# Performance work log

Measured on AMD Instinct MI355X. Metric: run time of the kernel, lower is better.

Reference implementation:

```python
import jax, jax.numpy as jnp
import numpy as np

N_HEAD = 16
WINDOW = 256


def setup_inputs() -> dict:
    key = jax.random.key(0)
    ks = jax.random.split(key, 3)
    B, S, D = 2, 2048, 1024
    x = jax.random.normal(ks[0], (B, S, D), dtype=jnp.float32)
    w_attn = jax.random.normal(ks[1], (D, 3 * D), dtype=jnp.float32) * 0.02
    b_attn = jnp.zeros((3 * D,), dtype=jnp.float32)
    w_proj = jax.random.normal(ks[2], (D, D), dtype=jnp.float32) * 0.02
    b_proj = jnp.zeros((D,), dtype=jnp.float32)
    return {"x": x, "w_attn": w_attn, "b_attn": b_attn, "w_proj": w_proj, "b_proj": b_proj}


def reference(x, w_attn, b_attn, w_proj, b_proj):
    B, S, D = x.shape
    hd = D // N_HEAD  # head dim
    scale = 1.0 / np.sqrt(hd).astype(np.float32)

    # fused QKV projection (Conv1D == linear on last dim)
    c = jnp.einsum('bsd,df->bsf', x, w_attn) + b_attn
    q, k, v = jnp.split(c, 3, axis=-1)

    def split_heads(t):  # [B,S,D] -> [B,H,S,hd]
        return t.reshape(B, S, N_HEAD, hd).transpose(0, 2, 1, 3)

    q, k, v = split_heads(q), split_heads(k), split_heads(v)
    present = jnp.stack([k, v], axis=1)  # [B,2,H,S,hd]

    # scores [B,H,S,S]
    w = jnp.einsum('bhqd,bhkd->bhqk', q, k) * scale

    # causal sliding-window mask
    q_pos = jnp.arange(S)[:, None]
    k_pos = jnp.arange(S)[None, :]
    mask = (k_pos <= q_pos) & (k_pos >= q_pos - WINDOW + 1)  # [S,S]
    w = jnp.where(mask[None, None], w, jnp.finfo(w.dtype).min)
    w = jax.nn.softmax(w, axis=-1)

    a = jnp.einsum('bhqk,bhkd->bhqd', w, v)
    a = a.transpose(0, 2, 1, 3).reshape(B, S, D)  # merge heads
    out = jnp.einsum('bsd,df->bsf', a, w_proj) + b_proj
    return out, present
```

## Files before the change

kernel.cpp:

```cpp
#include <hip/hip_runtime.h>
#include <cstdint>
#include <cstddef>

typedef __bf16 bf16x8 __attribute__((ext_vector_type(8)));
typedef float f32x4 __attribute__((ext_vector_type(4)));

#define MFMA16(a, b, c) __builtin_amdgcn_mfma_f32_16x16x32_bf16(a, b, c, 0, 0, 0)

static __device__ __forceinline__ bf16x8 ld_bf16x8(const __bf16* p) {
    return *reinterpret_cast<const bf16x8*>(p);
}

static __device__ __forceinline__ void async_cp16(const __bf16* g, __bf16* l) {
    __builtin_amdgcn_global_load_lds((const __attribute__((address_space(1))) void*)g,
                                     (__attribute__((address_space(3))) void*)l, 16, 0, 0);
}

template <int N>
static __device__ __forceinline__ void wait_vmcnt() {
    asm volatile("s_waitcnt vmcnt(%0)" ::"n"(N) : "memory");
}

__global__ void cvt_kernel(const float* __restrict__ src, __bf16* __restrict__ dst, int n8) {
    int i = blockIdx.x * blockDim.x + threadIdx.x;
    if (i >= n8) return;
    const float4* s4 = reinterpret_cast<const float4*>(src) + (size_t)i * 2;
    float4 a = s4[0], b = s4[1];
    bf16x8 o;
    o[0] = (__bf16)a.x; o[1] = (__bf16)a.y; o[2] = (__bf16)a.z; o[3] = (__bf16)a.w;
    o[4] = (__bf16)b.x; o[5] = (__bf16)b.y; o[6] = (__bf16)b.z; o[7] = (__bf16)b.w;
    reinterpret_cast<bf16x8*>(dst)[i] = o;
}

__global__ __launch_bounds__(256) void tcvt_kernel(const float* __restrict__ in,
                                                   __bf16* __restrict__ out, int K, int N) {
    __shared__ __bf16 T[64][72];
    const int k0 = blockIdx.y * 64, n0 = blockIdx.x * 64;
    const int t = threadIdx.x;
    const int col = (t & 15) << 2;
    const int rowb = t >> 4;
    #pragma unroll
    for (int i = 0; i < 4; i++) {
        int row = i * 16 + rowb;
        float4 v = *reinterpret_cast<const float4*>(&in[(size_t)(k0 + row) * N + n0 + col]);
        T[col + 0][row] = (__bf16)v.x;
        T[col + 1][row] = (__bf16)v.y;
        T[col + 2][row] = (__bf16)v.z;
        T[col + 3][row] = (__bf16)v.w;
    }
    __syncthreads();
    const int oc = (t & 7) << 3;
    const int orb = t >> 3;
    #pragma unroll
    for (int i = 0; i < 2; i++) {
        int r = i * 32 + orb;
        bf16x8 v = *reinterpret_cast<bf16x8*>(&T[r][oc]);
        *reinterpret_cast<bf16x8*>(&out[(size_t)(n0 + r) * K + k0 + oc]) = v;
    }
}

template <int BM, int BN, int WM, int WN>
__device__ __forceinline__ void mainloop2(const __bf16* __restrict__ A,
                                          const __bf16* __restrict__ Bt,
                                          int K, int row0, int col0,
                                          __bf16* lds,
                                          f32x4 (&acc)[BM / WM / 16][BN / WN / 16]) {
    constexpr int MR = BM / WM / 16, NR = BN / WN / 16;
    constexpr int AE = BM * 32;
    constexpr int BUFE = AE + BN * 32;
    constexpr int AI = BM / 16;
    constexpr int BI = BN / 16;
    constexpr int APW = AI / 8;
    constexpr int BPW = BI / 8;
    constexpr int BSPLIT = BI - BPW * 8;
    const int tid = threadIdx.x, l = tid & 63, w = tid >> 6;
    const int wm = w / WN, wn = w % WN;
    const int lr = l >> 2, lc = (l & 3) << 3;
    const int fr = l & 15, fc = (l >> 4) << 3;

    const size_t arow = (size_t)(row0 + lr) * K + lc;
    const size_t brow = (size_t)(col0 + lr) * K + lc;
    const int nt = K >> 5;

    auto stage = [&](int t, int buf) {
        const int k0 = t << 5;
        const int bb = buf * BUFE;
        #pragma unroll
        for (int j = 0; j < APW; j++) {
            const int mi = w * APW + j;
            async_cp16(A + arow + (size_t)mi * 16 * K + k0, lds + bb + mi * 512 + l * 8);
        }
        if (BSPLIT == 0) {
            #pragma unroll
            for (int j = 0; j < BPW; j++) {
                const int ni = w * BPW + j;
                async_cp16(Bt + brow + (size_t)ni * 16 * K + k0, lds + bb + AE + ni * 512 + l * 8);
            }
        } else if (w < BSPLIT) {
            #pragma unroll
            for (int j = 0; j < BPW + 1; j++) {
                const int ni = w * (BPW + 1) + j;
                async_cp16(Bt + brow + (size_t)ni * 16 * K + k0, lds + bb + AE + ni * 512 + l * 8);
            }
        } else {
            #pragma unroll
            for (int j = 0; j < BPW; j++) {
                const int ni = BSPLIT * (BPW + 1) + (w - BSPLIT) * BPW + j;
                async_cp16(Bt + brow + (size_t)ni * 16 * K + k0, lds + bb + AE + ni * 512 + l * 8);
            }
        }
    };

    stage(0, 0);
    stage(1, 1);

    const int aoff = (wm * (BM / WM) + fr) * 32 + fc;
    const int boff = AE + (wn * (BN / WN) + fr) * 32 + fc;

    int p = 0;
    for (int t = 0; t < nt; ++t) {
        if (t + 1 < nt) {
            if (BSPLIT != 0 && w < BSPLIT) wait_vmcnt<APW + BPW + 1>();
            else wait_vmcnt<APW + BPW>();
        } else {
            wait_vmcnt<0>();
        }
        __builtin_amdgcn_sched_barrier(0);
        __builtin_amdgcn_s_barrier();
        __builtin_amdgcn_sched_barrier(0);
        if (t + 2 < nt) {
            int p2 = p + 2; if (p2 >= 3) p2 -= 3;
            stage(t + 2, p2);
        }
        const int cb = p * BUFE;
        bf16x8 af[MR], bfv[NR];
        #pragma unroll
        for (int m = 0; m < MR; m++) af[m] = ld_bf16x8(&lds[cb + aoff + m * 512]);
        #pragma unroll
        for (int n = 0; n < NR; n++) bfv[n] = ld_bf16x8(&lds[cb + boff + n * 512]);
        __builtin_amdgcn_s_setprio(1);
        #pragma unroll
        for (int m = 0; m < MR; m++) {
            #pragma unroll
            for (int n = 0; n < NR; n++) {
                acc[m][n] = MFMA16(af[m], bfv[n], acc[m][n]);
            }
        }
        __builtin_amdgcn_s_setprio(0);
        asm volatile("s_waitcnt lgkmcnt(0)" ::: "memory");
        __builtin_amdgcn_sched_barrier(0);
        p = (p == 2) ? 0 : p + 1;
    }
}

__global__ __launch_bounds__(512, 2) void gemm_qkv_kernel(const __bf16* __restrict__ xb,
                                                          const __bf16* __restrict__ wabt,
                                                          const float* __restrict__ bias,
                                                          __bf16* __restrict__ qb,
                                                          __bf16* __restrict__ kb,
                                                          __bf16* __restrict__ vt,
                                                          float* __restrict__ present) {
    __shared__ __bf16 lds[3 * (256 * 32 + 192 * 32)];
    f32x4 acc[8][3] = {};
    const int row0 = blockIdx.y * 256, col0 = blockIdx.x * 192;
    mainloop2<256, 192, 2, 4>(xb, wabt, 1024, row0, col0, lds, acc);

    const int lane = threadIdx.x & 63, w = threadIdx.x >> 6;
    const int wm = w >> 2, wn = w & 3;
    #pragma unroll
    for (int n = 0; n < 3; n++) {
        int col = col0 + wn * 48 + n * 16 + (lane & 15);
        int part = col >> 10;
        int hh = (col >> 6) & 15;
        int dd = col & 63;
        float bv = bias[col];
        #pragma unroll
        for (int m = 0; m < 8; m++) {
            #pragma unroll
            for (int r = 0; r < 4; r++) {
                int row = row0 + wm * 128 + m * 16 + ((lane >> 4) << 2) + r;
                int bb = row >> 11, ss = row & 2047;
                float val = acc[m][n][r] + bv;
                size_t qi = (((size_t)(bb * 16 + hh)) * 2048 + ss) * 64 + dd;
                if (part == 0) {
                    qb[qi] = (__bf16)val;
                } else if (part == 1) {
                    kb[qi] = (__bf16)val;
                    present[(((size_t)((bb * 2 + 0) * 16 + hh)) * 2048 + ss) * 64 + dd] = val;
                } else {
                    vt[(((size_t)(bb * 16 + hh)) * 64 + dd) * 2048 + ss] = (__bf16)val;
                    present[(((size_t)((bb * 2 + 1) * 16 + hh)) * 2048 + ss) * 64 + dd] = val;
                }
            }
        }
    }
}

__global__ __launch_bounds__(512, 2) void gemm_proj_kernel(const __bf16* __restrict__ ab,
                                                           const __bf16* __restrict__ wpbt,
                                                           const float* __restrict__ bias,
                                                           float* __restrict__ out) {
    __shared__ __bf16 lds[3 * (128 * 32 + 128 * 32)];
    f32x4 acc[2][4] = {};
    const int row0 = blockIdx.y * 128, col0 = blockIdx.x * 128;
    mainloop2<128, 128, 4, 2>(ab, wpbt, 1024, row0, col0, lds, acc);

    const int lane = threadIdx.x & 63, w = threadIdx.x >> 6;
    const int wm = w >> 1, wn = w & 1;
    #pragma unroll
    for (int n = 0; n < 4; n++) {
        int col = col0 + wn * 64 + n * 16 + (lane & 15);
        float bv = bias[col];
        #pragma unroll
        for (int m = 0; m < 2; m++) {
            #pragma unroll
            for (int r = 0; r < 4; r++) {
                int row = row0 + wm * 32 + m * 16 + ((lane >> 4) << 2) + r;
                out[(size_t)row * 1024 + col] = acc[m][n][r] + bv;
            }
        }
    }
}

__global__ __launch_bounds__(256) void attn_kernel(const __bf16* __restrict__ qb,
                                                   const __bf16* __restrict__ kb,
                                                   const __bf16* __restrict__ vtb,
                                                   __bf16* __restrict__ ab) {
    __shared__ __bf16 Pls[4][16 * 40];
    const int bh = blockIdx.x >> 5;
    const int qt = blockIdx.x & 31;
    const int lane = threadIdx.x & 63, wid = threadIdx.x >> 6;
    const int q0w = qt * 64 + wid * 16;

    const __bf16* Qh = qb + (size_t)bh * 2048 * 64;
    const __bf16* Kh = kb + (size_t)bh * 2048 * 64;
    const __bf16* Vt = vtb + (size_t)bh * 64 * 2048;
    __bf16* Pw = &Pls[wid][0];

    bf16x8 qf[2];
    {
        int qr = q0w + (lane & 15);
        const __bf16* qp = Qh + (size_t)qr * 64 + ((lane >> 4) << 3);
        qf[0] = ld_bf16x8(qp);
        qf[1] = ld_bf16x8(qp + 32);
    }

    f32x4 o[4];
    #pragma unroll
    for (int dt = 0; dt < 4; dt++) o[dt] = (f32x4){0.f, 0.f, 0.f, 0.f};
    float mrun[4] = {-1e30f, -1e30f, -1e30f, -1e30f};
    float srun[4] = {0.f, 0.f, 0.f, 0.f};

    const float scale = 0.125f;
    int klo = q0w - 255;
    int kt0 = klo > 0 ? (klo & ~31) : 0;

    for (int kt = kt0; kt <= q0w + 15; kt += 32) {
        f32x4 s[2];
        #pragma unroll
        for (int kc = 0; kc < 2; kc++) {
            int krow = kt + kc * 16 + (lane & 15);
            const __bf16* kp = Kh + (size_t)krow * 64 + ((lane >> 4) << 3);
            bf16x8 kf0 = ld_bf16x8(kp);
            bf16x8 kf1 = ld_bf16x8(kp + 32);
            f32x4 a = (f32x4){0.f, 0.f, 0.f, 0.f};
            a = MFMA16(qf[0], kf0, a);
            a = MFMA16(qf[1], kf1, a);
            s[kc] = a;
        }
        float p0v[4], p1v[4], factor[4];
        #pragma unroll
        for (int r = 0; r < 4; r++) {
            int q = q0w + ((lane >> 4) << 2) + r;
            int k0i = kt + (lane & 15);
            int k1i = k0i + 16;
            bool ok0 = (k0i <= q) && (k0i > q - 256);
            bool ok1 = (k1i <= q) && (k1i > q - 256);
            float s0 = ok0 ? s[0][r] * scale : -1e30f;
            float s1 = ok1 ? s[1][r] * scale : -1e30f;
            float mx = fmaxf(s0, s1);
            #pragma unroll
            for (int off = 1; off < 16; off <<= 1) mx = fmaxf(mx, __shfl_xor(mx, off));
            float mn = fmaxf(mrun[r], mx);
            float f = __expf(mrun[r] - mn);
            float p0 = ok0 ? __expf(s0 - mn) : 0.f;
            float p1 = ok1 ? __expf(s1 - mn) : 0.f;
            float ps = p0 + p1;
            #pragma unroll
            for (int off = 1; off < 16; off <<= 1) ps += __shfl_xor(ps, off);
            srun[r] = srun[r] * f + ps;
            mrun[r] = mn;
            factor[r] = f;
            p0v[r] = p0;
            p1v[r] = p1;
        }
        #pragma unroll
        for (int dt = 0; dt < 4; dt++) {
            #pragma unroll
            for (int r = 0; r < 4; r++) o[dt][r] *= factor[r];
        }
        #pragma unroll
        for (int r = 0; r < 4; r++) {
            int qrow = ((lane >> 4) << 2) + r;
            Pw[qrow * 40 + (lane & 15)] = (__bf16)p0v[r];
            Pw[qrow * 40 + 16 + (lane & 15)] = (__bf16)p1v[r];
        }
        asm volatile("s_waitcnt lgkmcnt(0)" ::: "memory");
        bf16x8 pf = ld_bf16x8(&Pw[(lane & 15) * 40 + ((lane >> 4) << 3)]);
        #pragma unroll
        for (int dt = 0; dt < 4; dt++) {
            bf16x8 vf = ld_bf16x8(&Vt[(size_t)(dt * 16 + (lane & 15)) * 2048 + kt + ((lane >> 4) << 3)]);
            o[dt] = MFMA16(pf, vf, o[dt]);
        }
    }

    const int bb = bh >> 4, hh = bh & 15;
    #pragma unroll
    for (int r = 0; r < 4; r++) {
        int q = q0w + ((lane >> 4) << 2) + r;
        float inv = 1.f / srun[r];
        size_t base = ((size_t)bb * 2048 + q) * 1024 + hh * 64;
        #pragma unroll
        for (int dt = 0; dt < 4; dt++) {
            ab[base + dt * 16 + (lane & 15)] = (__bf16)(o[dt][r] * inv);
        }
    }
}

extern "C" void kernel_launch(void* const* d_in, const int* in_sizes, int n_in,
                              void* d_out, int out_size, void* d_ws, size_t ws_size,
                              hipStream_t stream) {
    const float* x = (const float*)d_in[0];
    const float* w_attn = (const float*)d_in[1];
    const float* b_attn = (const float*)d_in[2];
    const float* w_proj = (const float*)d_in[3];
    const float* b_proj = (const float*)d_in[4];

    float* out = (float*)d_out;
    float* present = out + (size_t)2 * 2048 * 1024;

    char* w = (char*)d_ws;
    __bf16* xb   = (__bf16*)(w);
    __bf16* wabt = (__bf16*)(w + 8388608);
    __bf16* wpbt = (__bf16*)(w + 14680064);
    __bf16* qb   = (__bf16*)(w + 16777216);
    __bf16* kb   = (__bf16*)(w + 25165824);
    __bf16* vt   = (__bf16*)(w + 33554432);
    __bf16* ab   = xb;

    cvt_kernel<<<2048, 256, 0, stream>>>(x, xb, 524288);
    tcvt_kernel<<<dim3(48, 16), 256, 0, stream>>>(w_attn, wabt, 1024, 3072);
    tcvt_kernel<<<dim3(16, 16), 256, 0, stream>>>(w_proj, wpbt, 1024, 1024);

    gemm_qkv_kernel<<<dim3(16, 16), 512, 0, stream>>>(xb, wabt, b_attn, qb, kb, vt, present);

    attn_kernel<<<1024, 256, 0, stream>>>(qb, kb, vt, ab);

    gemm_proj_kernel<<<dim3(8, 32), 512, 0, stream>>>(ab, wpbt, b_proj, out);
}
```

Baseline: 124.0 us.

## Rewrite QKV GEMM mainloop with 256x256 tiles, swizzled LDS and interleaved staging

Replaces the QKV projection GEMM mainloop with a new 256x256 tile loop that works on 64-wide K tiles split into two 32-wide halves and double-buffers them in LDS. Async global-to-LDS copies are interleaved between MFMA phases, and the LDS layout uses an XOR swizzle to avoid bank conflicts. The grid becomes 1D with 192 blocks remapped for L2 locality, so each block's columns fall within a single Q/K/V part. This aims to cut pipeline stalls and LDS conflicts and raise MFMA utilisation, but it adds many barriers and fewer, larger blocks, which could hurt occupancy or wave balance.

```diff
diff --git a/kernel.cpp b/kernel.cpp
--- a/kernel.cpp
+++ b/kernel.cpp
@@ -19,6 +19,12 @@
 template <int N>
 static __device__ __forceinline__ void wait_vmcnt() {
     asm volatile("s_waitcnt vmcnt(%0)" ::"n"(N) : "memory");
+}
+
+static __device__ __forceinline__ void barrier_pinned() {
+    __builtin_amdgcn_sched_barrier(0);
+    __builtin_amdgcn_s_barrier();
+    __builtin_amdgcn_sched_barrier(0);
 }
 
 __global__ void cvt_kernel(const float* __restrict__ src, __bf16* __restrict__ dst, int n8) {
@@ -56,6 +62,179 @@
         int r = i * 32 + orb;
         bf16x8 v = *reinterpret_cast<bf16x8*>(&T[r][oc]);
         *reinterpret_cast<bf16x8*>(&out[(size_t)(n0 + r) * K + k0 + oc]) = v;
+    }
+}
+
+
+template <int BUF, int KS, int MH>
+static __device__ __forceinline__ void ldA(const __bf16* lds, int aRow, int ch, bf16x8 (&af)[4]) {
+    #pragma unroll
+    for (int mi = 0; mi < 4; mi++)
+        af[mi] = ld_bf16x8(&lds[BUF * 32768 + KS * 8192 + (aRow + (MH * 4 + mi) * 16) * 32 + ch * 8]);
+}
+
+template <int BUF, int KS>
+static __device__ __forceinline__ void ldB(const __bf16* lds, int bRow, int ch, bf16x8 (&bf)[4]) {
+    #pragma unroll
+    for (int n = 0; n < 4; n++)
+        bf[n] = ld_bf16x8(&lds[BUF * 32768 + 16384 + KS * 8192 + (bRow + n * 16) * 32 + ch * 8]);
+}
+
+template <int MH>
+static __device__ __forceinline__ void mm16(const bf16x8 (&af)[4], const bf16x8 (&bf)[4],
+                                            f32x4 (&acc)[8][4]) {
+    __builtin_amdgcn_s_setprio(1);
+    #pragma unroll
+    for (int mi = 0; mi < 4; mi++) {
+        #pragma unroll
+        for (int n = 0; n < 4; n++) {
+            acc[MH * 4 + mi][n] = MFMA16(af[mi], bf[n], acc[MH * 4 + mi][n]);
+        }
+    }
+    __builtin_amdgcn_s_setprio(0);
+}
+
+__device__ __forceinline__ void mloop8(const __bf16* __restrict__ A,
+                                       const __bf16* __restrict__ Bt,
+                                       int K, int row0, int col0,
+                                       __bf16* lds, f32x4 (&acc)[8][4]) {
+    const int tid = threadIdx.x, l = tid & 63, w = tid >> 6;
+    const int wm = w >> 2, wn = w & 3;
+    const int fr = l & 15;
+    const int ch = (l >> 4) ^ ((fr >> 1) & 3);
+    const int NT = K >> 6;
+
+    const int g0 = tid, g1 = tid + 512;
+    const int r0s = g0 >> 2, c0 = (((g0 & 3) ^ ((r0s >> 1) & 3)) << 3);
+    const int r1s = g1 >> 2, c1 = (((g1 & 3) ^ ((r1s >> 1) & 3)) << 3);
+    const int d0 = g0 * 8, d1 = g1 * 8;
+
+    const int aRow = wm * 128 + fr;
+    const int bRow = wn * 64 + fr;
+
+    auto stg = [&](const __bf16* M, int rb, int ktile, int ksh, int dstoff) {
+        const __bf16* base = M + (size_t)ktile * 64 + ksh * 32;
+        async_cp16(base + (size_t)(rb + r0s) * K + c0, lds + dstoff + d0);
+        async_cp16(base + (size_t)(rb + r1s) * K + c1, lds + dstoff + d1);
+    };
+
+    stg(Bt, col0, 0, 0, 16384);
+    stg(A,  row0, 0, 0, 0);
+    stg(Bt, col0, 0, 1, 16384 + 8192);
+    stg(A,  row0, 0, 1, 8192);
+    stg(Bt, col0, 1, 0, 32768 + 16384);
+    stg(A,  row0, 1, 0, 32768);
+    stg(Bt, col0, 1, 1, 32768 + 16384 + 8192);
+    wait_vmcnt<6>();
+    barrier_pinned();
+
+    bf16x8 af[4], bf[4];
+    const int NI = NT >> 1;
+    for (int i = 0; i < NI; ++i) {
+        const int t0 = 2 * i, t1 = 2 * i + 1;
+        const bool s0 = (t0 + 2) < NT, s1 = (t1 + 2) < NT;
+
+        ldA<0, 0, 0>(lds, aRow, ch, af);
+        ldB<0, 0>(lds, bRow, ch, bf);
+        stg(A, row0, t1, 1, 32768 + 8192);
+        barrier_pinned();
+        mm16<0>(af, bf, acc);
+        barrier_pinned();
+        ldA<0, 0, 1>(lds, aRow, ch, af);
+        if (s0) stg(Bt, col0, t0 + 2, 0, 16384);
+        barrier_pinned();
+        mm16<1>(af, bf, acc);
+        barrier_pinned();
+        ldA<0, 1, 0>(lds, aRow, ch, af);
+        ldB<0, 1>(lds, bRow, ch, bf);
+        if (s0) stg(A, row0, t0 + 2, 0, 0);
+        barrier_pinned();
+        mm16<0>(af, bf, acc);
+        barrier_pinned();
+        ldA<0, 1, 1>(lds, aRow, ch, af);
+        if (s0) {
+            stg(Bt, col0, t0 + 2, 1, 16384 + 8192);
+            wait_vmcnt<6>();
+        } else {
+            wait_vmcnt<0>();
+        }
+        barrier_pinned();
+        mm16<1>(af, bf, acc);
+        barrier_pinned();
+        ldA<1, 0, 0>(lds, aRow, ch, af);
+        ldB<1, 0>(lds, bRow, ch, bf);
+        if (s0) stg(A, row0, t0 + 2, 1, 8192);
+        barrier_pinned();
+        mm16<0>(af, bf, acc);
+        barrier_pinned();
+        ldA<1, 0, 1>(lds, aRow, ch, af);
+        if (s1) stg(Bt, col0, t1 + 2, 0, 32768 + 16384);
+        barrier_pinned();
+        mm16<1>(af, bf, acc);
+        barrier_pinned();
+        ldA<1, 1, 0>(lds, aRow, ch, af);
+        ldB<1, 1>(lds, bRow, ch, bf);
+        if (s1) stg(A, row0, t1 + 2, 0, 32768);
+        barrier_pinned();
+        mm16<0>(af, bf, acc);
+        barrier_pinned();
+        ldA<1, 1, 1>(lds, aRow, ch, af);
+        if (s1) {
+            stg(Bt, col0, t1 + 2, 1, 32768 + 16384 + 8192);
+            wait_vmcnt<6>();
+        } else {
+            wait_vmcnt<0>();
+        }
+        barrier_pinned();
+        mm16<1>(af, bf, acc);
+        barrier_pinned();
+    }
+}
+
+__global__ __launch_bounds__(512, 2) void gemm_qkv_kernel(const __bf16* __restrict__ xb,
+                                                          const __bf16* __restrict__ wabt,
+                                                          const float* __restrict__ bias,
+                                                          __bf16* __restrict__ qb,
+                                                          __bf16* __restrict__ kb,
+                                                          __bf16* __restrict__ vt,
+                                                          float* __restrict__ present) {
+    __shared__ __bf16 lds[2 * 32768];
+    f32x4 acc[8][4] = {};
+
+    const int wg = (blockIdx.x & 7) * 24 + (blockIdx.x >> 3);
+    const int by = wg & 15, bx = wg >> 4;
+    const int row0 = by * 256, col0 = bx * 256;
+
+    mloop8(xb, wabt, 1024, row0, col0, lds, acc);
+
+    const int l = threadIdx.x & 63, w = threadIdx.x >> 6;
+    const int wm = w >> 2, wn = w & 3;
+    const int part = col0 >> 10;
+    #pragma unroll
+    for (int n = 0; n < 4; n++) {
+        int col = col0 + wn * 64 + n * 16 + (l & 15);
+        int hh = (col >> 6) & 15;
+        int dd = col & 63;
+        float bv = bias[col];
+        #pragma unroll
+        for (int m = 0; m < 8; m++) {
+            #pragma unroll
+            for (int r = 0; r < 4; r++) {
+                int row = row0 + wm * 128 + m * 16 + ((l >> 4) << 2) + r;
+                int bb = row >> 11, ss = row & 2047;
+                float val = acc[m][n][r] + bv;
+                size_t qi = (((size_t)(bb * 16 + hh)) * 2048 + ss) * 64 + dd;
+                if (part == 0) {
+                    qb[qi] = (__bf16)val;
+                } else if (part == 1) {
+                    kb[qi] = (__bf16)val;
+                    present[(((size_t)((bb * 2 + 0) * 16 + hh)) * 2048 + ss) * 64 + dd] = val;
+                } else {
+                    vt[(((size_t)(bb * 16 + hh)) * 64 + dd) * 2048 + ss] = (__bf16)val;
+                    present[(((size_t)((bb * 2 + 1) * 16 + hh)) * 2048 + ss) * 64 + dd] = val;
+                }
+            }
+        }
     }
 }
 
@@ -72,7 +251,6 @@
     constexpr int BI = BN / 16;
     constexpr int APW = AI / 8;
     constexpr int BPW = BI / 8;
-    constexpr int BSPLIT = BI - BPW * 8;
     const int tid = threadIdx.x, l = tid & 63, w = tid >> 6;
     const int wm = w / WN, wn = w % WN;
     const int lr = l >> 2, lc = (l & 3) << 3;
@@ -90,24 +268,10 @@
             const int mi = w * APW + j;
             async_cp16(A + arow + (size_t)mi * 16 * K + k0, lds + bb + mi * 512 + l * 8);
         }
-        if (BSPLIT == 0) {
-            #pragma unroll
-            for (int j = 0; j < BPW; j++) {
-                const int ni = w * BPW + j;
-                async_cp16(Bt + brow + (size_t)ni * 16 * K + k0, lds + bb + AE + ni * 512 + l * 8);
-            }
-        } else if (w < BSPLIT) {
-            #pragma unroll
-            for (int j = 0; j < BPW + 1; j++) {
-                const int ni = w * (BPW + 1) + j;
-                async_cp16(Bt + brow + (size_t)ni * 16 * K + k0, lds + bb + AE + ni * 512 + l * 8);
-            }
-        } else {
-            #pragma unroll
-            for (int j = 0; j < BPW; j++) {
-                const int ni = BSPLIT * (BPW + 1) + (w - BSPLIT) * BPW + j;
-                async_cp16(Bt + brow + (size_t)ni * 16 * K + k0, lds + bb + AE + ni * 512 + l * 8);
-            }
+        #pragma unroll
+        for (int j = 0; j < BPW; j++) {
+            const int ni = w * BPW + j;
+            async_cp16(Bt + brow + (size_t)ni * 16 * K + k0, lds + bb + AE + ni * 512 + l * 8);
         }
     };
 
@@ -120,14 +284,11 @@
     int p = 0;
     for (int t = 0; t < nt; ++t) {
         if (t + 1 < nt) {
-            if (BSPLIT != 0 && w < BSPLIT) wait_vmcnt<APW + BPW + 1>();
-            else wait_vmcnt<APW + BPW>();
+            wait_vmcnt<APW + BPW>();
         } else {
             wait_vmcnt<0>();
         }
-        __builtin_amdgcn_sched_barrier(0);
-        __builtin_amdgcn_s_barrier();
-        __builtin_amdgcn_sched_barrier(0);
+        barrier_pinned();
         if (t + 2 < nt) {
             int p2 = p + 2; if (p2 >= 3) p2 -= 3;
             stage(t + 2, p2);
@@ -150,49 +311,6 @@
         asm volatile("s_waitcnt lgkmcnt(0)" ::: "memory");
         __builtin_amdgcn_sched_barrier(0);
         p = (p == 2) ? 0 : p + 1;
-    }
-}
-
-__global__ __launch_bounds__(512, 2) void gemm_qkv_kernel(const __bf16* __restrict__ xb,
-                                                          const __bf16* __restrict__ wabt,
-                                                          const float* __restrict__ bias,
-                                                          __bf16* __restrict__ qb,
-                                                          __bf16* __restrict__ kb,
-                                                          __bf16* __restrict__ vt,
-                                                          float* __restrict__ present) {
-    __shared__ __bf16 lds[3 * (256 * 32 + 192 * 32)];
-    f32x4 acc[8][3] = {};
-    const int row0 = blockIdx.y * 256, col0 = blockIdx.x * 192;
-    mainloop2<256, 192, 2, 4>(xb, wabt, 1024, row0, col0, lds, acc);
-
-    const int lane = threadIdx.x & 63, w = threadIdx.x >> 6;
-    const int wm = w >> 2, wn = w & 3;
-    #pragma unroll
-    for (int n = 0; n < 3; n++) {
-        int col = col0 + wn * 48 + n * 16 + (lane & 15);
-        int part = col >> 10;
-        int hh = (col >> 6) & 15;
-        int dd = col & 63;
-        float bv = bias[col];
-        #pragma unroll
-        for (int m = 0; m < 8; m++) {
-            #pragma unroll
-            for (int r = 0; r < 4; r++) {
-                int row = row0 + wm * 128 + m * 16 + ((lane >> 4) << 2) + r;
-                int bb = row >> 11, ss = row & 2047;
-                float val = acc[m][n][r] + bv;
-                size_t qi = (((size_t)(bb * 16 + hh)) * 2048 + ss) * 64 + dd;
-                if (part == 0) {
-                    qb[qi] = (__bf16)val;
-                } else if (part == 1) {
-                    kb[qi] = (__bf16)val;
-                    present[(((size_t)((bb * 2 + 0) * 16 + hh)) * 2048 + ss) * 64 + dd] = val;
-                } else {
-                    vt[(((size_t)(bb * 16 + hh)) * 64 + dd) * 2048 + ss] = (__bf16)val;
-                    present[(((size_t)((bb * 2 + 1) * 16 + hh)) * 2048 + ss) * 64 + dd] = val;
-                }
-            }
-        }
     }
 }
 
@@ -352,7 +470,7 @@
     tcvt_kernel<<<dim3(48, 16), 256, 0, stream>>>(w_attn, wabt, 1024, 3072);
     tcvt_kernel<<<dim3(16, 16), 256, 0, stream>>>(w_proj, wpbt, 1024, 1024);
 
-    gemm_qkv_kernel<<<dim3(16, 16), 512, 0, stream>>>(xb, wabt, b_attn, qb, kb, vt, present);
+    gemm_qkv_kernel<<<192, 512, 0, stream>>>(xb, wabt, b_attn, qb, kb, vt, present);
 
     attn_kernel<<<1024, 256, 0, stream>>>(qb, kb, vt, ab);
 
```

Measured after the change: 129.4 us. 4.3% more time.
